# Kernel optimization log

Measured on AMD Instinct MI355X. Metric: run time of the kernel, lower is better.

Reference implementation:

```python
import jax, jax.numpy as jnp
import numpy as np

D_MODEL = 256
NHEAD = 8
HEAD_DIM = D_MODEL // NHEAD
CLIP = 10.0


def setup_inputs() -> dict:
    key = jax.random.key(0)
    k1, k2, k3, k4 = jax.random.split(key, 4)
    B, N = 4, 256
    nodes = jax.random.normal(k1, (B, N, D_MODEL), dtype=jnp.float32)
    edges = jax.random.normal(k2, (B, N, N, D_MODEL), dtype=jnp.float32)
    # torch nn.Linear default init: U(-1/sqrt(in), 1/sqrt(in))
    bound = 1.0 / np.sqrt(D_MODEL)
    W = jax.random.uniform(k3, (D_MODEL, D_MODEL), minval=-bound, maxval=bound, dtype=jnp.float32)
    b = jax.random.uniform(k4, (D_MODEL,), minval=-bound, maxval=bound, dtype=jnp.float32)
    return {"nodes": nodes, "edges": edges, "W": W, "b": b}


def reference(nodes, edges, W, b):
    B, N, _ = nodes.shape
    H, Dh = NHEAD, HEAD_DIM

    def proj(x):  # torch Linear: x @ W.T + b
        return x @ W.T + b

    # Node projections: the module applies the SAME linear to q, k, v
    node_p = proj(nodes).reshape(B, N, H, Dh)
    nq, nk, nv = node_p, node_p, node_p
    # Edge projections (same linear for q and k)
    edge_p = proj(edges).reshape(B, N, N, H, Dh)
    eq, ek = edge_p, edge_p

    query = eq + nq[:, :, None, :, :]   # (B,N,N,H,Dh)
    key = ek + nk[:, None, :, :, :]     # (B,N,N,H,Dh)
    scores = jnp.einsum('bijhd,bijhd->bhij', query, key) / np.sqrt(Dh).astype(np.float32)
    scores = CLIP * jnp.tanh(scores)
    attn = jax.nn.softmax(scores, axis=-1)  # (B,H,N,N)
    # output = attn @ values (values transposed to (B,H,N,Dh))
    out = jnp.einsum('bhij,bjhd->bihd', attn, nv).reshape(B, N, D_MODEL)
    out = proj(out)
    return (out, attn)
```

## Files before the change

kernel.cpp:

```cpp
#include <hip/hip_runtime.h>
#include <hip/hip_bf16.h>
#include <math.h>

typedef short short8 __attribute__((ext_vector_type(8)));
typedef float f32x4 __attribute__((ext_vector_type(4)));

__device__ __forceinline__ unsigned short f2bf(float x) {
    unsigned u = __float_as_uint(x);
    u += 0x7FFF + ((u >> 16) & 1);
    return (unsigned short)(u >> 16);
}
__device__ __forceinline__ float bf2f(unsigned short h) {
    return __uint_as_float(((unsigned)h) << 16);
}

__device__ __forceinline__ void cvtpair(float f0, float f1, unsigned& hw, unsigned& lw) {
    __hip_bfloat162 h2 = __float22bfloat162_rn(float2{f0, f1});
    unsigned hu = *(unsigned*)&h2;
    float r0 = f0 - __uint_as_float(hu << 16);
    float r1 = f1 - __uint_as_float(hu & 0xFFFF0000u);
    __hip_bfloat162 l2 = __float22bfloat162_rn(float2{r0, r1});
    hw = hu;
    lw = *(unsigned*)&l2;
}

__device__ __forceinline__ void cvt8(const float4 a, const float4 b, short8& hi, short8& lo) {
    union { unsigned u[4]; short8 s; } H, L;
    cvtpair(a.x, a.y, H.u[0], L.u[0]);
    cvtpair(a.z, a.w, H.u[1], L.u[1]);
    cvtpair(b.x, b.y, H.u[2], L.u[2]);
    cvtpair(b.z, b.w, H.u[3], L.u[3]);
    hi = H.s; lo = L.s;
}

__device__ __forceinline__ float tanh10(float y) {
    float e = __expf(2.f * y);
    return 10.f * (e - 1.f) / (e + 1.f);
}

#define GLDS16(gp, lp)                                                        \
    __builtin_amdgcn_global_load_lds(                                         \
        (const __attribute__((address_space(1))) void*)(gp),                  \
        (__attribute__((address_space(3))) void*)(lp), 16, 0, 0)

__global__ __launch_bounds__(256) void k_prep(const float* __restrict__ W,
                                              float* __restrict__ Wt,
                                              unsigned short* __restrict__ Whi,
                                              unsigned short* __restrict__ Wlo) {
    int d = blockIdx.x, k = threadIdx.x;
    float w = W[d * 256 + k];
    Wt[k * 256 + d] = w;
    unsigned short hi = f2bf(w);
    int s  = (k >> 3) & 3;
    int sp = s ^ ((d >> 1) & 3);
    int idx = d * 256 + (k & ~31) + sp * 8 + (k & 7);
    Whi[idx] = hi;
    Wlo[idx] = f2bf(w - bf2f(hi));
}

__global__ __launch_bounds__(256) void k_node_proj(const float* __restrict__ nodes,
                                                   const float* __restrict__ Wt,
                                                   const float* __restrict__ bias,
                                                   float* __restrict__ np_) {
    int row = blockIdx.x;
    int d = threadIdx.x;
    __shared__ float xl[256];
    xl[d] = nodes[row * 256 + d];
    __syncthreads();
    float a[8] = {0.f, 0.f, 0.f, 0.f, 0.f, 0.f, 0.f, 0.f};
#pragma unroll 4
    for (int k = 0; k < 256; k += 8) {
#pragma unroll
        for (int q = 0; q < 8; ++q)
            a[q] = fmaf(xl[k + q], Wt[(k + q) * 256 + d], a[q]);
    }
    np_[row * 256 + d] =
        bias[d] + ((a[0] + a[1]) + (a[2] + a[3])) + ((a[4] + a[5]) + (a[6] + a[7]));
}

__global__ __launch_bounds__(256) void k_edge_mfma(const float* __restrict__ edges,
                                                   const unsigned short* __restrict__ Whi,
                                                   const unsigned short* __restrict__ Wlo,
                                                   const float* __restrict__ bias,
                                                   const float* __restrict__ np_,
                                                   float* __restrict__ attn) {
    __shared__ unsigned short Wbuf[2][2][128 * 32];
    __shared__ float npi[128];
    __shared__ float sc[4][128];

    const int t = threadIdx.x;
    const int w = t >> 6, l = t & 63;

    const int L = (blockIdx.x & 7) * 512 + (blockIdx.x >> 3);
    const int tile = L >> 1, half = L & 1;
    const int m0 = tile * 128;
    const int bb = m0 >> 16;
    const int ii = (m0 >> 8) & 255;
    const int j0 = m0 & 255;
    const int n0 = half * 128;

    const int col = l & 15, g = l >> 4;
    const int wrow = l >> 2, wq = l & 3;

    if (t < 32)
        ((float4*)npi)[t] = ((const float4*)(np_ + (size_t)(bb * 256 + ii) * 256 + n0))[t];

    f32x4 acc[2][8];
#pragma unroll
    for (int mt = 0; mt < 2; ++mt)
#pragma unroll
        for (int nt = 0; nt < 8; ++nt) acc[mt][nt] = (f32x4){0.f, 0.f, 0.f, 0.f};

    const float* ea0 = edges + (size_t)(m0 + w * 32 + col) * 256 + g * 8;
    const float* ea1 = ea0 + 16 * 256;

    const size_t wg0 = (size_t)(n0 + w * 32 + wrow) * 256 + wq * 8;
    const size_t wg1 = wg0 + 16 * 256;

    float4 e0a = *(const float4*)(ea0);
    float4 e0b = *(const float4*)(ea0 + 4);
    float4 e1a = *(const float4*)(ea1);
    float4 e1b = *(const float4*)(ea1 + 4);
    GLDS16(Whi + wg0, &Wbuf[0][0][(w * 32) * 32]);
    GLDS16(Wlo + wg0, &Wbuf[0][1][(w * 32) * 32]);
    GLDS16(Whi + wg1, &Wbuf[0][0][(w * 32 + 16) * 32]);
    GLDS16(Wlo + wg1, &Wbuf[0][1][(w * 32 + 16) * 32]);

    short8 Ah[2], Al[2];
    cvt8(e0a, e0b, Ah[0], Al[0]);
    cvt8(e1a, e1b, Ah[1], Al[1]);
    __syncthreads();

    const int swb = (g ^ ((col >> 1) & 3)) << 3;

#pragma unroll 2
    for (int kc = 0; kc < 8; ++kc) {
        float4 p0a, p0b, p1a, p1b;
        if (kc < 7) {
            const int nb = (kc + 1) & 1;
            const size_t kofs = (size_t)(kc + 1) * 32;
            GLDS16(Whi + wg0 + kofs, &Wbuf[nb][0][(w * 32) * 32]);
            GLDS16(Wlo + wg0 + kofs, &Wbuf[nb][1][(w * 32) * 32]);
            GLDS16(Whi + wg1 + kofs, &Wbuf[nb][0][(w * 32 + 16) * 32]);
            GLDS16(Wlo + wg1 + kofs, &Wbuf[nb][1][(w * 32 + 16) * 32]);
            p0a = *(const float4*)(ea0 + (kc + 1) * 32);
            p0b = *(const float4*)(ea0 + (kc + 1) * 32 + 4);
            p1a = *(const float4*)(ea1 + (kc + 1) * 32);
            p1b = *(const float4*)(ea1 + (kc + 1) * 32 + 4);
        }
        const unsigned short* bh = &Wbuf[kc & 1][0][0] + col * 32 + swb;
        const unsigned short* bl = &Wbuf[kc & 1][1][0] + col * 32 + swb;
#pragma unroll
        for (int nt = 0; nt < 8; ++nt) {
            short8 Bh = *(const short8*)(bh + nt * 512);
            short8 Bl = *(const short8*)(bl + nt * 512);
            acc[0][nt] = __builtin_amdgcn_mfma_f32_16x16x32_bf16(Ah[0], Bh, acc[0][nt], 0, 0, 0);
            acc[1][nt] = __builtin_amdgcn_mfma_f32_16x16x32_bf16(Ah[1], Bh, acc[1][nt], 0, 0, 0);
            acc[0][nt] = __builtin_amdgcn_mfma_f32_16x16x32_bf16(Ah[0], Bl, acc[0][nt], 0, 0, 0);
            acc[1][nt] = __builtin_amdgcn_mfma_f32_16x16x32_bf16(Ah[1], Bl, acc[1][nt], 0, 0, 0);
            acc[0][nt] = __builtin_amdgcn_mfma_f32_16x16x32_bf16(Al[0], Bh, acc[0][nt], 0, 0, 0);
            acc[1][nt] = __builtin_amdgcn_mfma_f32_16x16x32_bf16(Al[1], Bh, acc[1][nt], 0, 0, 0);
        }
        if (kc < 7) {
            cvt8(p0a, p0b, Ah[0], Al[0]);
            cvt8(p1a, p1b, Ah[1], Al[1]);
        }
        __syncthreads();
    }

    const float isq = 0.17677669529663687f;
    float bv[8], nv[8];
#pragma unroll
    for (int nt = 0; nt < 8; ++nt) {
        int dl = nt * 16 + col;
        bv[nt] = bias[n0 + dl];
        nv[nt] = npi[dl];
    }
#pragma unroll
    for (int mt = 0; mt < 2; ++mt) {
#pragma unroll
        for (int r = 0; r < 4; ++r) {
            int el = w * 32 + mt * 16 + g * 4 + r;
            int j = j0 + el;
            const float* npj = np_ + (size_t)(bb * 256 + j) * 256 + n0;
            float p, s0 = 0.f, s1 = 0.f, s2 = 0.f, s3 = 0.f;
            p = acc[mt][0][r] + bv[0]; s0 += (p + nv[0]) * (p + npj[col]);
            p = acc[mt][1][r] + bv[1]; s0 += (p + nv[1]) * (p + npj[16 + col]);
            p = acc[mt][2][r] + bv[2]; s1 += (p + nv[2]) * (p + npj[32 + col]);
            p = acc[mt][3][r] + bv[3]; s1 += (p + nv[3]) * (p + npj[48 + col]);
            p = acc[mt][4][r] + bv[4]; s2 += (p + nv[4]) * (p + npj[64 + col]);
            p = acc[mt][5][r] + bv[5]; s2 += (p + nv[5]) * (p + npj[80 + col]);
            p = acc[mt][6][r] + bv[6]; s3 += (p + nv[6]) * (p + npj[96 + col]);
            p = acc[mt][7][r] + bv[7]; s3 += (p + nv[7]) * (p + npj[112 + col]);
#pragma unroll
            for (int m = 1; m < 16; m <<= 1) {
                s0 += __shfl_xor(s0, m, 64);
                s1 += __shfl_xor(s1, m, 64);
                s2 += __shfl_xor(s2, m, 64);
                s3 += __shfl_xor(s3, m, 64);
            }
            if (col == 0) {
                sc[0][el] = tanh10(s0 * isq);
                sc[1][el] = tanh10(s1 * isq);
                sc[2][el] = tanh10(s2 * isq);
                sc[3][el] = tanh10(s3 * isq);
            }
        }
    }
    __syncthreads();
    if (t < 128) {
        int hl = t >> 5, q = t & 31;
        float4 v = *(float4*)&sc[hl][q * 4];
        *(float4*)(attn + (((size_t)(bb * 8 + half * 4 + hl) * 256 + ii) << 8) + j0 + q * 4) = v;
    }
}

__global__ __launch_bounds__(256) void k_softmax(float* __restrict__ attn) {
    int row = (blockIdx.x * 256 + threadIdx.x) >> 6;
    int lane = threadIdx.x & 63;
    float4* rowp = (float4*)(attn + (size_t)row * 256);
    float4 v = rowp[lane];
    float m = fmaxf(fmaxf(v.x, v.y), fmaxf(v.z, v.w));
#pragma unroll
    for (int s = 1; s < 64; s <<= 1) m = fmaxf(m, __shfl_xor(m, s, 64));
    v.x = __expf(v.x - m); v.y = __expf(v.y - m);
    v.z = __expf(v.z - m); v.w = __expf(v.w - m);
    float sum = v.x + v.y + v.z + v.w;
#pragma unroll
    for (int s = 1; s < 64; s <<= 1) sum += __shfl_xor(sum, s, 64);
    float inv = 1.f / sum;
    v.x *= inv; v.y *= inv; v.z *= inv; v.w *= inv;
    rowp[lane] = v;
}

__global__ __launch_bounds__(256) void k_out(const float* __restrict__ attn,
                                             const float* __restrict__ np_,
                                             const float* __restrict__ Wt,
                                             const float* __restrict__ bias,
                                             float* __restrict__ out) {
    int bi = blockIdx.x;
    int bb = bi >> 8, ii = bi & 255;
    int d = threadIdx.x;
    __shared__ float at[8 * 256];
    __shared__ float xl[256];
#pragma unroll
    for (int s = 0; s < 2; ++s) {
        int idx = d + s * 256;
        int h = idx >> 6, q = idx & 63;
        ((float4*)at)[idx] =
            ((const float4*)(attn + ((size_t)(bb * 8 + h) * 256 + ii) * 256))[q];
    }
    __syncthreads();
    int h = d >> 5;
    const float* npb = np_ + (size_t)bb * 65536 + d;
    const float* ath = at + h * 256;
    float a[8] = {0.f, 0.f, 0.f, 0.f, 0.f, 0.f, 0.f, 0.f};
#pragma unroll 2
    for (int j = 0; j < 256; j += 8) {
#pragma unroll
        for (int q = 0; q < 8; ++q)
            a[q] = fmaf(ath[j + q], npb[(size_t)(j + q) * 256], a[q]);
    }
    xl[d] = ((a[0] + a[1]) + (a[2] + a[3])) + ((a[4] + a[5]) + (a[6] + a[7]));
    __syncthreads();
    float c[8] = {bias[d], 0.f, 0.f, 0.f, 0.f, 0.f, 0.f, 0.f};
#pragma unroll 2
    for (int k = 0; k < 256; k += 8) {
#pragma unroll
        for (int q = 0; q < 8; ++q)
            c[q] = fmaf(xl[k + q], Wt[(k + q) * 256 + d], c[q]);
    }
    out[bi * 256 + d] =
        ((c[0] + c[1]) + (c[2] + c[3])) + ((c[4] + c[5]) + (c[6] + c[7]));
}

extern "C" void kernel_launch(void* const* d_in, const int* in_sizes, int n_in,
                              void* d_out, int out_size, void* d_ws, size_t ws_size,
                              hipStream_t stream) {
    (void)in_sizes; (void)n_in; (void)out_size; (void)ws_size;
    const float* nodes = (const float*)d_in[0];
    const float* edges = (const float*)d_in[1];
    const float* W     = (const float*)d_in[2];
    const float* bias  = (const float*)d_in[3];

    float* out  = (float*)d_out;
    float* attn = out + 262144;

    float* np_ = (float*)d_ws;
    float* Wt  = np_ + 262144;
    unsigned short* Whi = (unsigned short*)(Wt + 65536);
    unsigned short* Wlo = Whi + 65536;

    hipLaunchKernelGGL(k_prep,      dim3(256),  dim3(256), 0, stream, W, Wt, Whi, Wlo);
    hipLaunchKernelGGL(k_node_proj, dim3(1024), dim3(256), 0, stream, nodes, Wt, bias, np_);
    hipLaunchKernelGGL(k_edge_mfma, dim3(4096), dim3(256), 0, stream, edges, Whi, Wlo, bias, np_, attn);
    hipLaunchKernelGGL(k_softmax,   dim3(2048), dim3(256), 0, stream, attn);
    hipLaunchKernelGGL(k_out,       dim3(1024), dim3(256), 0, stream, attn, np_, Wt, bias, out);
}
```

Measured before the change: 512.9 us.

## Fuse softmax into edge MFMA kernel with full-row tiles and direct-register weights

Each block of the edge projection kernel now covers a full row of 256 j values for one (b,i) and one half of the heads. That lets it apply the softmax in-kernel, so the separate softmax kernel and its extra read and write of attn are removed. The LDS-staged, swizzled double-buffered weight tiles are replaced by short8 loads straight from global memory into registers, prefetched one step ahead, which removes the per-k-chunk barriers. The price is doubled accumulator registers (4x8 tiles), weight reads now served from cache instead of LDS, and a min-2-blocks launch bound that may cause spills.

```diff
diff --git a/kernel.cpp b/kernel.cpp
--- a/kernel.cpp
+++ b/kernel.cpp
@@ -38,11 +38,6 @@
     return 10.f * (e - 1.f) / (e + 1.f);
 }
 
-#define GLDS16(gp, lp)                                                        \
-    __builtin_amdgcn_global_load_lds(                                         \
-        (const __attribute__((address_space(1))) void*)(gp),                  \
-        (__attribute__((address_space(3))) void*)(lp), 16, 0, 0)
-
 __global__ __launch_bounds__(256) void k_prep(const float* __restrict__ W,
                                               float* __restrict__ Wt,
                                               unsigned short* __restrict__ Whi,
@@ -51,11 +46,8 @@
     float w = W[d * 256 + k];
     Wt[k * 256 + d] = w;
     unsigned short hi = f2bf(w);
-    int s  = (k >> 3) & 3;
-    int sp = s ^ ((d >> 1) & 3);
-    int idx = d * 256 + (k & ~31) + sp * 8 + (k & 7);
-    Whi[idx] = hi;
-    Wlo[idx] = f2bf(w - bf2f(hi));
+    Whi[d * 256 + k] = hi;
+    Wlo[d * 256 + k] = f2bf(w - bf2f(hi));
 }
 
 __global__ __launch_bounds__(256) void k_node_proj(const float* __restrict__ nodes,
@@ -78,95 +70,77 @@
         bias[d] + ((a[0] + a[1]) + (a[2] + a[3])) + ((a[4] + a[5]) + (a[6] + a[7]));
 }
 
-__global__ __launch_bounds__(256) void k_edge_mfma(const float* __restrict__ edges,
-                                                   const unsigned short* __restrict__ Whi,
-                                                   const unsigned short* __restrict__ Wlo,
-                                                   const float* __restrict__ bias,
-                                                   const float* __restrict__ np_,
-                                                   float* __restrict__ attn) {
-    __shared__ unsigned short Wbuf[2][2][128 * 32];
+__global__ __launch_bounds__(256, 2) void k_edge_mfma(const float* __restrict__ edges,
+                                                      const unsigned short* __restrict__ Whi,
+                                                      const unsigned short* __restrict__ Wlo,
+                                                      const float* __restrict__ bias,
+                                                      const float* __restrict__ np_,
+                                                      float* __restrict__ attn) {
     __shared__ float npi[128];
-    __shared__ float sc[4][128];
+    __shared__ float sc[4][256];
 
     const int t = threadIdx.x;
     const int w = t >> 6, l = t & 63;
-
-    const int L = (blockIdx.x & 7) * 512 + (blockIdx.x >> 3);
+    const int col = l & 15, g = l >> 4;
+
+    const int p = blockIdx.x;
+    const int L = (p & 7) * 256 + (p >> 3);
     const int tile = L >> 1, half = L & 1;
-    const int m0 = tile * 128;
-    const int bb = m0 >> 16;
-    const int ii = (m0 >> 8) & 255;
-    const int j0 = m0 & 255;
+    const int bb = tile >> 8, ii = tile & 255;
     const int n0 = half * 128;
-
-    const int col = l & 15, g = l >> 4;
-    const int wrow = l >> 2, wq = l & 3;
 
     if (t < 32)
         ((float4*)npi)[t] = ((const float4*)(np_ + (size_t)(bb * 256 + ii) * 256 + n0))[t];
 
-    f32x4 acc[2][8];
-#pragma unroll
-    for (int mt = 0; mt < 2; ++mt)
+    f32x4 acc[4][8];
+#pragma unroll
+    for (int mt = 0; mt < 4; ++mt)
 #pragma unroll
         for (int nt = 0; nt < 8; ++nt) acc[mt][nt] = (f32x4){0.f, 0.f, 0.f, 0.f};
 
-    const float* ea0 = edges + (size_t)(m0 + w * 32 + col) * 256 + g * 8;
-    const float* ea1 = ea0 + 16 * 256;
-
-    const size_t wg0 = (size_t)(n0 + w * 32 + wrow) * 256 + wq * 8;
-    const size_t wg1 = wg0 + 16 * 256;
-
-    float4 e0a = *(const float4*)(ea0);
-    float4 e0b = *(const float4*)(ea0 + 4);
-    float4 e1a = *(const float4*)(ea1);
-    float4 e1b = *(const float4*)(ea1 + 4);
-    GLDS16(Whi + wg0, &Wbuf[0][0][(w * 32) * 32]);
-    GLDS16(Wlo + wg0, &Wbuf[0][1][(w * 32) * 32]);
-    GLDS16(Whi + wg1, &Wbuf[0][0][(w * 32 + 16) * 32]);
-    GLDS16(Wlo + wg1, &Wbuf[0][1][(w * 32 + 16) * 32]);
-
-    short8 Ah[2], Al[2];
-    cvt8(e0a, e0b, Ah[0], Al[0]);
-    cvt8(e1a, e1b, Ah[1], Al[1]);
-    __syncthreads();
-
-    const int swb = (g ^ ((col >> 1) & 3)) << 3;
-
-#pragma unroll 2
+    const float* ea = edges + ((size_t)((bb * 256 + ii) * 256 + w * 64 + col)) * 256 + g * 8;
+    const int lidx = col * 256 + g * 8;
+
+    float4 e[4][2];
+#pragma unroll
+    for (int mt = 0; mt < 4; ++mt) {
+        e[mt][0] = *(const float4*)(ea + mt * 4096);
+        e[mt][1] = *(const float4*)(ea + mt * 4096 + 4);
+    }
+    short8 Bh = *(const short8*)(Whi + (size_t)(n0 * 256) + lidx);
+    short8 Bl = *(const short8*)(Wlo + (size_t)(n0 * 256) + lidx);
+
+    short8 Ah[4], Al[4];
+
     for (int kc = 0; kc < 8; ++kc) {
-        float4 p0a, p0b, p1a, p1b;
+#pragma unroll
+        for (int mt = 0; mt < 4; ++mt)
+            cvt8(e[mt][0], e[mt][1], Ah[mt], Al[mt]);
         if (kc < 7) {
-            const int nb = (kc + 1) & 1;
-            const size_t kofs = (size_t)(kc + 1) * 32;
-            GLDS16(Whi + wg0 + kofs, &Wbuf[nb][0][(w * 32) * 32]);
-            GLDS16(Wlo + wg0 + kofs, &Wbuf[nb][1][(w * 32) * 32]);
-            GLDS16(Whi + wg1 + kofs, &Wbuf[nb][0][(w * 32 + 16) * 32]);
-            GLDS16(Wlo + wg1 + kofs, &Wbuf[nb][1][(w * 32 + 16) * 32]);
-            p0a = *(const float4*)(ea0 + (kc + 1) * 32);
-            p0b = *(const float4*)(ea0 + (kc + 1) * 32 + 4);
-            p1a = *(const float4*)(ea1 + (kc + 1) * 32);
-            p1b = *(const float4*)(ea1 + (kc + 1) * 32 + 4);
+#pragma unroll
+            for (int mt = 0; mt < 4; ++mt) {
+                e[mt][0] = *(const float4*)(ea + (kc + 1) * 32 + mt * 4096);
+                e[mt][1] = *(const float4*)(ea + (kc + 1) * 32 + mt * 4096 + 4);
+            }
         }
-        const unsigned short* bh = &Wbuf[kc & 1][0][0] + col * 32 + swb;
-        const unsigned short* bl = &Wbuf[kc & 1][1][0] + col * 32 + swb;
 #pragma unroll
         for (int nt = 0; nt < 8; ++nt) {
-            short8 Bh = *(const short8*)(bh + nt * 512);
-            short8 Bl = *(const short8*)(bl + nt * 512);
-            acc[0][nt] = __builtin_amdgcn_mfma_f32_16x16x32_bf16(Ah[0], Bh, acc[0][nt], 0, 0, 0);
-            acc[1][nt] = __builtin_amdgcn_mfma_f32_16x16x32_bf16(Ah[1], Bh, acc[1][nt], 0, 0, 0);
-            acc[0][nt] = __builtin_amdgcn_mfma_f32_16x16x32_bf16(Ah[0], Bl, acc[0][nt], 0, 0, 0);
-            acc[1][nt] = __builtin_amdgcn_mfma_f32_16x16x32_bf16(Ah[1], Bl, acc[1][nt], 0, 0, 0);
-            acc[0][nt] = __builtin_amdgcn_mfma_f32_16x16x32_bf16(Al[0], Bh, acc[0][nt], 0, 0, 0);
-            acc[1][nt] = __builtin_amdgcn_mfma_f32_16x16x32_bf16(Al[1], Bh, acc[1][nt], 0, 0, 0);
+            short8 cBh = Bh, cBl = Bl;
+            const int nt2 = (nt + 1) & 7;
+            const int kc2 = (nt == 7) ? kc + 1 : kc;
+            const size_t wofs = (size_t)((n0 + nt2 * 16) * 256 + kc2 * 32);
+            Bh = *(const short8*)(Whi + wofs + lidx);
+            Bl = *(const short8*)(Wlo + wofs + lidx);
+#pragma unroll
+            for (int mt = 0; mt < 4; ++mt) {
+                acc[mt][nt] = __builtin_amdgcn_mfma_f32_16x16x32_bf16(Ah[mt], cBh, acc[mt][nt], 0, 0, 0);
+                acc[mt][nt] = __builtin_amdgcn_mfma_f32_16x16x32_bf16(Ah[mt], cBl, acc[mt][nt], 0, 0, 0);
+                acc[mt][nt] = __builtin_amdgcn_mfma_f32_16x16x32_bf16(Al[mt], cBh, acc[mt][nt], 0, 0, 0);
+            }
         }
-        if (kc < 7) {
-            cvt8(p0a, p0b, Ah[0], Al[0]);
-            cvt8(p1a, p1b, Ah[1], Al[1]);
-        }
-        __syncthreads();
-    }
+    }
+
+    __syncthreads();
 
     const float isq = 0.17677669529663687f;
     float bv[8], nv[8];
@@ -177,21 +151,20 @@
         nv[nt] = npi[dl];
     }
 #pragma unroll
-    for (int mt = 0; mt < 2; ++mt) {
+    for (int mt = 0; mt < 4; ++mt) {
 #pragma unroll
         for (int r = 0; r < 4; ++r) {
-            int el = w * 32 + mt * 16 + g * 4 + r;
-            int j = j0 + el;
-            const float* npj = np_ + (size_t)(bb * 256 + j) * 256 + n0;
-            float p, s0 = 0.f, s1 = 0.f, s2 = 0.f, s3 = 0.f;
-            p = acc[mt][0][r] + bv[0]; s0 += (p + nv[0]) * (p + npj[col]);
-            p = acc[mt][1][r] + bv[1]; s0 += (p + nv[1]) * (p + npj[16 + col]);
-            p = acc[mt][2][r] + bv[2]; s1 += (p + nv[2]) * (p + npj[32 + col]);
-            p = acc[mt][3][r] + bv[3]; s1 += (p + nv[3]) * (p + npj[48 + col]);
-            p = acc[mt][4][r] + bv[4]; s2 += (p + nv[4]) * (p + npj[64 + col]);
-            p = acc[mt][5][r] + bv[5]; s2 += (p + nv[5]) * (p + npj[80 + col]);
-            p = acc[mt][6][r] + bv[6]; s3 += (p + nv[6]) * (p + npj[96 + col]);
-            p = acc[mt][7][r] + bv[7]; s3 += (p + nv[7]) * (p + npj[112 + col]);
+            int el = w * 64 + mt * 16 + g * 4 + r;
+            const float* npj = np_ + (size_t)(bb * 256 + el) * 256 + n0;
+            float pp, s0 = 0.f, s1 = 0.f, s2 = 0.f, s3 = 0.f;
+            pp = acc[mt][0][r] + bv[0]; s0 += (pp + nv[0]) * (pp + npj[col]);
+            pp = acc[mt][1][r] + bv[1]; s0 += (pp + nv[1]) * (pp + npj[16 + col]);
+            pp = acc[mt][2][r] + bv[2]; s1 += (pp + nv[2]) * (pp + npj[32 + col]);
+            pp = acc[mt][3][r] + bv[3]; s1 += (pp + nv[3]) * (pp + npj[48 + col]);
+            pp = acc[mt][4][r] + bv[4]; s2 += (pp + nv[4]) * (pp + npj[64 + col]);
+            pp = acc[mt][5][r] + bv[5]; s2 += (pp + nv[5]) * (pp + npj[80 + col]);
+            pp = acc[mt][6][r] + bv[6]; s3 += (pp + nv[6]) * (pp + npj[96 + col]);
+            pp = acc[mt][7][r] + bv[7]; s3 += (pp + nv[7]) * (pp + npj[112 + col]);
 #pragma unroll
             for (int m = 1; m < 16; m <<= 1) {
                 s0 += __shfl_xor(s0, m, 64);
@@ -208,29 +181,21 @@
         }
     }
     __syncthreads();
-    if (t < 128) {
-        int hl = t >> 5, q = t & 31;
-        float4 v = *(float4*)&sc[hl][q * 4];
-        *(float4*)(attn + (((size_t)(bb * 8 + half * 4 + hl) * 256 + ii) << 8) + j0 + q * 4) = v;
-    }
-}
-
-__global__ __launch_bounds__(256) void k_softmax(float* __restrict__ attn) {
-    int row = (blockIdx.x * 256 + threadIdx.x) >> 6;
-    int lane = threadIdx.x & 63;
-    float4* rowp = (float4*)(attn + (size_t)row * 256);
-    float4 v = rowp[lane];
-    float m = fmaxf(fmaxf(v.x, v.y), fmaxf(v.z, v.w));
-#pragma unroll
-    for (int s = 1; s < 64; s <<= 1) m = fmaxf(m, __shfl_xor(m, s, 64));
-    v.x = __expf(v.x - m); v.y = __expf(v.y - m);
-    v.z = __expf(v.z - m); v.w = __expf(v.w - m);
-    float sum = v.x + v.y + v.z + v.w;
-#pragma unroll
-    for (int s = 1; s < 64; s <<= 1) sum += __shfl_xor(sum, s, 64);
-    float inv = 1.f / sum;
-    v.x *= inv; v.y *= inv; v.z *= inv; v.w *= inv;
-    rowp[lane] = v;
+
+    {
+        float4 v = *(float4*)&sc[w][l * 4];
+        float m = fmaxf(fmaxf(v.x, v.y), fmaxf(v.z, v.w));
+#pragma unroll
+        for (int s = 1; s < 64; s <<= 1) m = fmaxf(m, __shfl_xor(m, s, 64));
+        v.x = __expf(v.x - m); v.y = __expf(v.y - m);
+        v.z = __expf(v.z - m); v.w = __expf(v.w - m);
+        float sum = v.x + v.y + v.z + v.w;
+#pragma unroll
+        for (int s = 1; s < 64; s <<= 1) sum += __shfl_xor(sum, s, 64);
+        float inv = 1.f / sum;
+        v.x *= inv; v.y *= inv; v.z *= inv; v.w *= inv;
+        *(float4*)(attn + (((size_t)(bb * 8 + half * 4 + w) * 256 + ii) << 8) + l * 4) = v;
+    }
 }
 
 __global__ __launch_bounds__(256) void k_out(const float* __restrict__ attn,
@@ -293,7 +258,6 @@
 
     hipLaunchKernelGGL(k_prep,      dim3(256),  dim3(256), 0, stream, W, Wt, Whi, Wlo);
     hipLaunchKernelGGL(k_node_proj, dim3(1024), dim3(256), 0, stream, nodes, Wt, bias, np_);
-    hipLaunchKernelGGL(k_edge_mfma, dim3(4096), dim3(256), 0, stream, edges, Whi, Wlo, bias, np_, attn);
-    hipLaunchKernelGGL(k_softmax,   dim3(2048), dim3(256), 0, stream, attn);
+    hipLaunchKernelGGL(k_edge_mfma, dim3(2048), dim3(256), 0, stream, edges, Whi, Wlo, bias, np_, attn);
     hipLaunchKernelGGL(k_out,       dim3(1024), dim3(256), 0, stream, attn, np_, Wt, bias, out);
 }
```

New measurement: 543.0 us. 1.06x slower.
